# Optimization experiments

Measured on AMD Instinct MI355X. Metric: run time of the kernel, lower is better.

Reference implementation:

```python
import jax, jax.numpy as jnp
import numpy as np

EPS = 1e-6

def _phi(x):
    # elu(x) + 1 feature map
    return jax.nn.elu(x) + 1.0

def setup_inputs() -> dict:
    key = jax.random.key(0)
    kq, kk, kv = jax.random.split(key, 3)
    N, L, S, H, D, M = 8, 4096, 4096, 8, 64, 64
    queries = jax.random.normal(kq, (N, L, H, D), dtype=jnp.float32)
    keys = jax.random.normal(kk, (N, S, H, D), dtype=jnp.float32)
    values = jax.random.normal(kv, (N, S, H, M), dtype=jnp.float32)
    key_mask = jnp.ones((N, S), dtype=jnp.float32)  # key_lengths.float_matrix
    return {"queries": queries, "keys": keys, "values": values, "key_mask": key_mask}

def reference(queries, keys, values, key_mask):
    Q = _phi(queries)                                   # [N,L,H,D]
    K = _phi(keys) * key_mask[:, :, None, None]         # [N,S,H,D]
    KV = jnp.einsum('nshd,nshm->nhmd', K, values)       # [N,H,M,D]
    Z = 1.0 / (jnp.einsum('nlhd,nhd->nlh', Q, K.sum(axis=1)) + EPS)  # [N,L,H]
    V = jnp.einsum('nlhd,nhmd,nlh->nlhm', Q, KV, Z)     # [N,L,H,M]
    return V
```

## Files before the change

kernel.cpp:

```cpp
#include <hip/hip_runtime.h>


#define SLEN 4096
#define LLEN 4096
#define NHTOT 64
#define HD   512
#define NSPLIT 16
#define EPSF 1e-6f

__device__ __forceinline__ float phi(float x) {
    return x > 0.0f ? x + 1.0f : __expf(x);
}

__device__ __forceinline__ void fma4(float4& a, float s, const float4& b) {
    a.x = fmaf(s, b.x, a.x);
    a.y = fmaf(s, b.y, a.y);
    a.z = fmaf(s, b.z, a.z);
    a.w = fmaf(s, b.w, a.w);
}

__global__ __launch_bounds__(256)
void la_phase1(const float* __restrict__ Kg, const float* __restrict__ Vg,
               const float* __restrict__ maskg,
               float* __restrict__ KVp, float* __restrict__ Ksump) {
    __shared__ float kb[64 * 68];
    __shared__ float vb[64 * 64];
    __shared__ float ksb[16 * 64];

    const int tid  = threadIdx.x;
    const int w    = tid >> 6;
    const int lane = tid & 63;
    const int nh   = blockIdx.y;
    const int n    = nh >> 3;
    const int h    = nh & 7;
    const int sp   = blockIdx.x;

    const int sr = tid >> 4;
    const int c4 = (tid & 15) * 4;
    const int wd = w & 1, wm = w >> 1;
    const int d0 = wd * 32 + (lane & 7) * 4;
    const int m0 = wm * 32 + (lane >> 3) * 4;

    const size_t base = (size_t)n * SLEN * HD + (size_t)h * 64;
    const float* mrow = maskg + (size_t)n * SLEN;
    const int sblock = sp * 256;

    float4 acc[4];
    #pragma unroll
    for (int i = 0; i < 4; ++i) acc[i] = make_float4(0.f, 0.f, 0.f, 0.f);
    float4 ksp = make_float4(0.f, 0.f, 0.f, 0.f);

    for (int t = 0; t < 4; ++t) {
        const int srow0 = sblock + t * 64;
        __syncthreads();
        #pragma unroll
        for (int u = 0; u < 4; ++u) {
            const int row = sr + u * 16;
            const int s   = srow0 + row;
            const size_t g = base + (size_t)s * HD + c4;
            float4 kf = *(const float4*)(Kg + g);
            const float mm = mrow[s];
            kf.x = phi(kf.x) * mm;
            kf.y = phi(kf.y) * mm;
            kf.z = phi(kf.z) * mm;
            kf.w = phi(kf.w) * mm;
            ksp.x += kf.x; ksp.y += kf.y; ksp.z += kf.z; ksp.w += kf.w;
            *(float4*)&kb[row * 68 + c4] = kf;
            *(float4*)&vb[row * 64 + c4] = *(const float4*)(Vg + g);
        }
        __syncthreads();
        #pragma unroll 8
        for (int s = 0; s < 64; ++s) {
            const float4 k4 = *(const float4*)&kb[s * 68 + d0];
            const float4 v4 = *(const float4*)&vb[s * 64 + m0];
            fma4(acc[0], k4.x, v4);
            fma4(acc[1], k4.y, v4);
            fma4(acc[2], k4.z, v4);
            fma4(acc[3], k4.w, v4);
        }
    }

    float* outp = KVp + ((size_t)sp * NHTOT + nh) * 4096;
    #pragma unroll
    for (int di = 0; di < 4; ++di)
        *(float4*)&outp[(d0 + di) * 64 + m0] = acc[di];

    *(float4*)&ksb[sr * 64 + c4] = ksp;
    __syncthreads();
    if (tid < 64) {
        float ssum = 0.f;
        #pragma unroll
        for (int r = 0; r < 16; ++r) ssum += ksb[r * 64 + tid];
        Ksump[((size_t)sp * NHTOT + nh) * 64 + tid] = ssum;
    }
}

__global__ __launch_bounds__(256)
void la_reduce(const float* __restrict__ KVp, const float* __restrict__ Ksump,
               float* __restrict__ KVt, float* __restrict__ Ksum) {
    const int nh  = blockIdx.x;
    const int tid = threadIdx.x;
    #pragma unroll
    for (int j = 0; j < 4; ++j) {
        const int f = (j * 256 + tid) * 4;
        float4 a = make_float4(0.f, 0.f, 0.f, 0.f);
        #pragma unroll
        for (int s = 0; s < NSPLIT; ++s) {
            const float4 v = *(const float4*)&KVp[((size_t)s * NHTOT + nh) * 4096 + f];
            a.x += v.x; a.y += v.y; a.z += v.z; a.w += v.w;
        }
        *(float4*)&KVt[(size_t)nh * 4096 + f] = a;
    }
    if (tid < 64) {
        float a = 0.f;
        #pragma unroll
        for (int s = 0; s < NSPLIT; ++s)
            a += Ksump[((size_t)s * NHTOT + nh) * 64 + tid];
        Ksum[nh * 64 + tid] = a;
    }
}

__global__ __launch_bounds__(256)
void la_phase2(const float* __restrict__ Qg, const float* __restrict__ KVt,
               const float* __restrict__ Ksum, float* __restrict__ Og) {
    __shared__ float Qs[128 * 68];
    __shared__ float KVs[64 * 64];
    __shared__ float KSs[64];

    const int tid = threadIdx.x;
    const int nh  = blockIdx.y;
    const int n   = nh >> 3;
    const int h   = nh & 7;
    const int lbase = blockIdx.x * 128;

    #pragma unroll
    for (int j = 0; j < 4; ++j) {
        const int f = (j * 256 + tid) * 4;
        *(float4*)&KVs[f] = *(const float4*)&KVt[(size_t)nh * 4096 + f];
    }
    if (tid < 16) *(float4*)&KSs[tid * 4] = *(const float4*)&Ksum[nh * 64 + tid * 4];

    const int sr = tid >> 4;
    const int c4 = (tid & 15) * 4;
    #pragma unroll
    for (int u = 0; u < 8; ++u) {
        const int row = sr + u * 16;
        float4 q = *(const float4*)&Qg[((size_t)(n * LLEN + lbase + row) * 8 + h) * 64 + c4];
        q.x = phi(q.x); q.y = phi(q.y); q.z = phi(q.z); q.w = phi(q.w);
        *(float4*)&Qs[row * 68 + c4] = q;
    }
    __syncthreads();

    const int w    = tid >> 6;
    const int lane = tid & 63;
    const int ty   = lane >> 4;
    const int tx   = lane & 15;
    const int m0   = tx * 4;
    const int rb   = w * 32 + ty;

    float4 acc[8];
    float  den[8];
    #pragma unroll
    for (int i = 0; i < 8; ++i) {
        acc[i] = make_float4(0.f, 0.f, 0.f, 0.f);
        den[i] = 0.f;
    }

    for (int d4 = 0; d4 < 16; ++d4) {
        const float4 ks = *(const float4*)&KSs[d4 * 4];
        float4 q4[8];
        #pragma unroll
        for (int i = 0; i < 8; ++i)
            q4[i] = *(const float4*)&Qs[(rb + 4 * i) * 68 + d4 * 4];
        #pragma unroll
        for (int i = 0; i < 8; ++i) {
            den[i] = fmaf(q4[i].x, ks.x, den[i]);
            den[i] = fmaf(q4[i].y, ks.y, den[i]);
            den[i] = fmaf(q4[i].z, ks.z, den[i]);
            den[i] = fmaf(q4[i].w, ks.w, den[i]);
        }
        #pragma unroll
        for (int dk = 0; dk < 4; ++dk) {
            const float4 kv = *(const float4*)&KVs[(d4 * 4 + dk) * 64 + m0];
            #pragma unroll
            for (int i = 0; i < 8; ++i)
                fma4(acc[i], (&q4[i].x)[dk], kv);
        }
    }

    #pragma unroll
    for (int i = 0; i < 8; ++i) {
        const int l = lbase + rb + 4 * i;
        const float z = 1.0f / (den[i] + EPSF);
        float4 o = acc[i];
        o.x *= z; o.y *= z; o.z *= z; o.w *= z;
        *(float4*)&Og[((size_t)(n * LLEN + l) * 8 + h) * 64 + m0] = o;
    }
}

extern "C" void kernel_launch(void* const* d_in, const int* in_sizes, int n_in,
                              void* d_out, int out_size, void* d_ws, size_t ws_size,
                              hipStream_t stream) {
    const float* Q    = (const float*)d_in[0];
    const float* K    = (const float*)d_in[1];
    const float* V    = (const float*)d_in[2];
    const float* mask = (const float*)d_in[3];
    float* out = (float*)d_out;

    float* KVp   = (float*)d_ws;
    float* Ksump = KVp + (size_t)NSPLIT * NHTOT * 4096;
    float* KVt   = Ksump + (size_t)NSPLIT * NHTOT * 64;
    float* Ksum  = KVt + (size_t)NHTOT * 4096;

    dim3 g1(NSPLIT, NHTOT);
    la_phase1<<<g1, 256, 0, stream>>>(K, V, mask, KVp, Ksump);

    la_reduce<<<NHTOT, 256, 0, stream>>>(KVp, Ksump, KVt, Ksum);

    dim3 g2(LLEN / 128, NHTOT);
    la_phase2<<<g2, 256, 0, stream>>>(Q, KVt, Ksum, out);
}
```

Measured before the change: 255.1 us.

## Retile phase1 with per-wave S split and LDS reduction, widen reduce and phase2 tiles

Phase1 now has each wave own a 16-row slice of S and accumulate the full 64x64 KV tile with an 8x8 register block per thread. The four wave partials are combined through a two-step LDS tree reduction. The reduce kernel is flattened across 257 blocks so more of the GPU is busy. Phase2 processes 256 rows per block with 8x8 register tiles and a swizzled, half-depth Q staging buffer to cut LDS bank conflicts. The larger register tiles raise the FMA-per-load ratio but increase register pressure, and the phase2 grid shrinks to half as many blocks.

After: 292.0 us. +14.4%, slower.

```diff
diff --git a/kernel.cpp b/kernel.cpp
--- a/kernel.cpp
+++ b/kernel.cpp
@@ -19,13 +19,20 @@
     a.w = fmaf(s, b.w, a.w);
 }
 
+__device__ __forceinline__ void add4(float4& a, const float4& b) {
+    a.x += b.x; a.y += b.y; a.z += b.z; a.w += b.w;
+}
+
 __global__ __launch_bounds__(256)
 void la_phase1(const float* __restrict__ Kg, const float* __restrict__ Vg,
                const float* __restrict__ maskg,
                float* __restrict__ KVp, float* __restrict__ Ksump) {
-    __shared__ float kb[64 * 68];
-    __shared__ float vb[64 * 64];
-    __shared__ float ksb[16 * 64];
+    __shared__ float lds[9472];
+    float* kb  = lds;
+    float* vb  = lds + 4352;
+    float* ksb = lds + 8448;
+    float* Red0 = lds;
+    float* Red1 = lds + 4096;
 
     const int tid  = threadIdx.x;
     const int w    = tid >> 6;
@@ -37,17 +44,19 @@
 
     const int sr = tid >> 4;
     const int c4 = (tid & 15) * 4;
-    const int wd = w & 1, wm = w >> 1;
-    const int d0 = wd * 32 + (lane & 7) * 4;
-    const int m0 = wm * 32 + (lane >> 3) * 4;
+    const int d0 = (lane & 7) * 8;
+    const int m0 = (lane >> 3) * 8;
 
     const size_t base = (size_t)n * SLEN * HD + (size_t)h * 64;
     const float* mrow = maskg + (size_t)n * SLEN;
     const int sblock = sp * 256;
 
-    float4 acc[4];
+    float4 acc[8][2];
     #pragma unroll
-    for (int i = 0; i < 4; ++i) acc[i] = make_float4(0.f, 0.f, 0.f, 0.f);
+    for (int i = 0; i < 8; ++i) {
+        acc[i][0] = make_float4(0.f, 0.f, 0.f, 0.f);
+        acc[i][1] = make_float4(0.f, 0.f, 0.f, 0.f);
+    }
     float4 ksp = make_float4(0.f, 0.f, 0.f, 0.f);
 
     for (int t = 0; t < 4; ++t) {
@@ -69,69 +78,123 @@
             *(float4*)&vb[row * 64 + c4] = *(const float4*)(Vg + g);
         }
         __syncthreads();
-        #pragma unroll 8
-        for (int s = 0; s < 64; ++s) {
-            const float4 k4 = *(const float4*)&kb[s * 68 + d0];
-            const float4 v4 = *(const float4*)&vb[s * 64 + m0];
-            fma4(acc[0], k4.x, v4);
-            fma4(acc[1], k4.y, v4);
-            fma4(acc[2], k4.z, v4);
-            fma4(acc[3], k4.w, v4);
-        }
-    }
-
-    float* outp = KVp + ((size_t)sp * NHTOT + nh) * 4096;
-    #pragma unroll
-    for (int di = 0; di < 4; ++di)
-        *(float4*)&outp[(d0 + di) * 64 + m0] = acc[di];
-
+        #pragma unroll
+        for (int j = 0; j < 16; ++j) {
+            const int s = w * 16 + j;
+            const float4 ka = *(const float4*)&kb[s * 68 + d0];
+            const float4 kc = *(const float4*)&kb[s * 68 + d0 + 4];
+            const float4 va = *(const float4*)&vb[s * 64 + m0];
+            const float4 vc = *(const float4*)&vb[s * 64 + m0 + 4];
+            const float kk[8] = {ka.x, ka.y, ka.z, ka.w, kc.x, kc.y, kc.z, kc.w};
+            #pragma unroll
+            for (int di = 0; di < 8; ++di) {
+                fma4(acc[di][0], kk[di], va);
+                fma4(acc[di][1], kk[di], vc);
+            }
+        }
+    }
+
+    __syncthreads();
+    if (w == 2) {
+        #pragma unroll
+        for (int di = 0; di < 8; ++di) {
+            *(float4*)&Red0[(d0 + di) * 64 + m0]     = acc[di][0];
+            *(float4*)&Red0[(d0 + di) * 64 + m0 + 4] = acc[di][1];
+        }
+    }
+    if (w == 3) {
+        #pragma unroll
+        for (int di = 0; di < 8; ++di) {
+            *(float4*)&Red1[(d0 + di) * 64 + m0]     = acc[di][0];
+            *(float4*)&Red1[(d0 + di) * 64 + m0 + 4] = acc[di][1];
+        }
+    }
     *(float4*)&ksb[sr * 64 + c4] = ksp;
     __syncthreads();
+    if (w == 0) {
+        #pragma unroll
+        for (int di = 0; di < 8; ++di) {
+            const float4 a = *(const float4*)&Red0[(d0 + di) * 64 + m0];
+            const float4 b = *(const float4*)&Red0[(d0 + di) * 64 + m0 + 4];
+            add4(acc[di][0], a);
+            add4(acc[di][1], b);
+        }
+    }
+    if (w == 1) {
+        #pragma unroll
+        for (int di = 0; di < 8; ++di) {
+            const float4 a = *(const float4*)&Red1[(d0 + di) * 64 + m0];
+            const float4 b = *(const float4*)&Red1[(d0 + di) * 64 + m0 + 4];
+            add4(acc[di][0], a);
+            add4(acc[di][1], b);
+        }
+    }
     if (tid < 64) {
         float ssum = 0.f;
         #pragma unroll
         for (int r = 0; r < 16; ++r) ssum += ksb[r * 64 + tid];
         Ksump[((size_t)sp * NHTOT + nh) * 64 + tid] = ssum;
+    }
+    __syncthreads();
+    if (w == 1) {
+        #pragma unroll
+        for (int di = 0; di < 8; ++di) {
+            *(float4*)&Red0[(d0 + di) * 64 + m0]     = acc[di][0];
+            *(float4*)&Red0[(d0 + di) * 64 + m0 + 4] = acc[di][1];
+        }
+    }
+    __syncthreads();
+    if (w == 0) {
+        float* outp = KVp + ((size_t)sp * NHTOT + nh) * 4096;
+        #pragma unroll
+        for (int di = 0; di < 8; ++di) {
+            const float4 a = *(const float4*)&Red0[(d0 + di) * 64 + m0];
+            const float4 b = *(const float4*)&Red0[(d0 + di) * 64 + m0 + 4];
+            float4 o0 = acc[di][0], o1 = acc[di][1];
+            add4(o0, a);
+            add4(o1, b);
+            *(float4*)&outp[(d0 + di) * 64 + m0]     = o0;
+            *(float4*)&outp[(d0 + di) * 64 + m0 + 4] = o1;
+        }
     }
 }
 
 __global__ __launch_bounds__(256)
 void la_reduce(const float* __restrict__ KVp, const float* __restrict__ Ksump,
                float* __restrict__ KVt, float* __restrict__ Ksum) {
-    const int nh  = blockIdx.x;
     const int tid = threadIdx.x;
-    #pragma unroll
-    for (int j = 0; j < 4; ++j) {
-        const int f = (j * 256 + tid) * 4;
+    if (blockIdx.x < 256) {
+        const size_t f = ((size_t)blockIdx.x * 256 + tid) * 4;
         float4 a = make_float4(0.f, 0.f, 0.f, 0.f);
         #pragma unroll
-        for (int s = 0; s < NSPLIT; ++s) {
-            const float4 v = *(const float4*)&KVp[((size_t)s * NHTOT + nh) * 4096 + f];
-            a.x += v.x; a.y += v.y; a.z += v.z; a.w += v.w;
-        }
-        *(float4*)&KVt[(size_t)nh * 4096 + f] = a;
-    }
-    if (tid < 64) {
-        float a = 0.f;
-        #pragma unroll
-        for (int s = 0; s < NSPLIT; ++s)
-            a += Ksump[((size_t)s * NHTOT + nh) * 64 + tid];
-        Ksum[nh * 64 + tid] = a;
+        for (int sp = 0; sp < NSPLIT; ++sp)
+            add4(a, *(const float4*)&KVp[(size_t)sp * NHTOT * 4096 + f]);
+        *(float4*)&KVt[f] = a;
+    } else {
+        #pragma unroll
+        for (int j = 0; j < 4; ++j) {
+            const int c = (j * 256 + tid) * 4;
+            float4 a = make_float4(0.f, 0.f, 0.f, 0.f);
+            #pragma unroll
+            for (int sp = 0; sp < NSPLIT; ++sp)
+                add4(a, *(const float4*)&Ksump[sp * NHTOT * 64 + c]);
+            *(float4*)&Ksum[c] = a;
+        }
     }
 }
 
 __global__ __launch_bounds__(256)
 void la_phase2(const float* __restrict__ Qg, const float* __restrict__ KVt,
                const float* __restrict__ Ksum, float* __restrict__ Og) {
-    __shared__ float Qs[128 * 68];
-    __shared__ float KVs[64 * 64];
+    __shared__ float Qs[256 * 32];
+    __shared__ float KVs[4096];
     __shared__ float KSs[64];
 
     const int tid = threadIdx.x;
     const int nh  = blockIdx.y;
     const int n   = nh >> 3;
     const int h   = nh & 7;
-    const int lbase = blockIdx.x * 128;
+    const int lbase = blockIdx.x * 256;
 
     #pragma unroll
     for (int j = 0; j < 4; ++j) {
@@ -140,61 +203,79 @@
     }
     if (tid < 16) *(float4*)&KSs[tid * 4] = *(const float4*)&Ksum[nh * 64 + tid * 4];
 
-    const int sr = tid >> 4;
-    const int c4 = (tid & 15) * 4;
-    #pragma unroll
-    for (int u = 0; u < 8; ++u) {
-        const int row = sr + u * 16;
-        float4 q = *(const float4*)&Qg[((size_t)(n * LLEN + lbase + row) * 8 + h) * 64 + c4];
-        q.x = phi(q.x); q.y = phi(q.y); q.z = phi(q.z); q.w = phi(q.w);
-        *(float4*)&Qs[row * 68 + c4] = q;
-    }
-    __syncthreads();
-
     const int w    = tid >> 6;
     const int lane = tid & 63;
-    const int ty   = lane >> 4;
-    const int tx   = lane & 15;
-    const int m0   = tx * 4;
-    const int rb   = w * 32 + ty;
-
-    float4 acc[8];
+    const int ry   = lane >> 3;
+    const int tx   = lane & 7;
+    const int m0   = tx * 8;
+    const int rowb = w * 64 + ry;
+
+    const int sc   = tid & 7;
+    const int srow = tid >> 3;
+
+    float4 acc[8][2];
     float  den[8];
     #pragma unroll
     for (int i = 0; i < 8; ++i) {
-        acc[i] = make_float4(0.f, 0.f, 0.f, 0.f);
+        acc[i][0] = make_float4(0.f, 0.f, 0.f, 0.f);
+        acc[i][1] = make_float4(0.f, 0.f, 0.f, 0.f);
         den[i] = 0.f;
     }
 
-    for (int d4 = 0; d4 < 16; ++d4) {
-        const float4 ks = *(const float4*)&KSs[d4 * 4];
-        float4 q4[8];
-        #pragma unroll
-        for (int i = 0; i < 8; ++i)
-            q4[i] = *(const float4*)&Qs[(rb + 4 * i) * 68 + d4 * 4];
-        #pragma unroll
-        for (int i = 0; i < 8; ++i) {
-            den[i] = fmaf(q4[i].x, ks.x, den[i]);
-            den[i] = fmaf(q4[i].y, ks.y, den[i]);
-            den[i] = fmaf(q4[i].z, ks.z, den[i]);
-            den[i] = fmaf(q4[i].w, ks.w, den[i]);
-        }
-        #pragma unroll
-        for (int dk = 0; dk < 4; ++dk) {
-            const float4 kv = *(const float4*)&KVs[(d4 * 4 + dk) * 64 + m0];
-            #pragma unroll
-            for (int i = 0; i < 8; ++i)
-                fma4(acc[i], (&q4[i].x)[dk], kv);
+    for (int half = 0; half < 2; ++half) {
+        __syncthreads();
+        #pragma unroll
+        for (int p = 0; p < 8; ++p) {
+            const int row = srow + p * 32;
+            float4 q = *(const float4*)&Qg[((size_t)(n * LLEN + lbase + row) * 8 + h) * 64
+                                           + half * 32 + sc * 4];
+            q.x = phi(q.x); q.y = phi(q.y); q.z = phi(q.z); q.w = phi(q.w);
+            const int chunk = (sc + row) & 7;
+            *(float4*)&Qs[row * 32 + chunk * 4] = q;
+        }
+        __syncthreads();
+        #pragma unroll
+        for (int dq = 0; dq < 8; ++dq) {
+            const float4 ks = *(const float4*)&KSs[(half * 8 + dq) * 4];
+            float4 q4[8];
+            #pragma unroll
+            for (int i = 0; i < 8; ++i) {
+                const int row = rowb + 8 * i;
+                const int chunk = (dq + row) & 7;
+                q4[i] = *(const float4*)&Qs[row * 32 + chunk * 4];
+            }
+            #pragma unroll
+            for (int i = 0; i < 8; ++i) {
+                den[i] = fmaf(q4[i].x, ks.x, den[i]);
+                den[i] = fmaf(q4[i].y, ks.y, den[i]);
+                den[i] = fmaf(q4[i].z, ks.z, den[i]);
+                den[i] = fmaf(q4[i].w, ks.w, den[i]);
+            }
+            #pragma unroll
+            for (int dk = 0; dk < 4; ++dk) {
+                const int d = half * 32 + dq * 4 + dk;
+                const float4 kv0 = *(const float4*)&KVs[d * 64 + m0];
+                const float4 kv1 = *(const float4*)&KVs[d * 64 + m0 + 4];
+                #pragma unroll
+                for (int i = 0; i < 8; ++i) {
+                    const float qs = (&q4[i].x)[dk];
+                    fma4(acc[i][0], qs, kv0);
+                    fma4(acc[i][1], qs, kv1);
+                }
+            }
         }
     }
 
     #pragma unroll
     for (int i = 0; i < 8; ++i) {
-        const int l = lbase + rb + 4 * i;
+        const int l = lbase + rowb + 8 * i;
         const float z = 1.0f / (den[i] + EPSF);
-        float4 o = acc[i];
-        o.x *= z; o.y *= z; o.z *= z; o.w *= z;
-        *(float4*)&Og[((size_t)(n * LLEN + l) * 8 + h) * 64 + m0] = o;
+        float4 o0 = acc[i][0], o1 = acc[i][1];
+        o0.x *= z; o0.y *= z; o0.z *= z; o0.w *= z;
+        o1.x *= z; o1.y *= z; o1.z *= z; o1.w *= z;
+        float* op = Og + ((size_t)(n * LLEN + l) * 8 + h) * 64 + m0;
+        *(float4*)&op[0] = o0;
+        *(float4*)&op[4] = o1;
     }
 }
 
@@ -215,8 +296,8 @@
     dim3 g1(NSPLIT, NHTOT);
     la_phase1<<<g1, 256, 0, stream>>>(K, V, mask, KVp, Ksump);
 
-    la_reduce<<<NHTOT, 256, 0, stream>>>(KVp, Ksump, KVt, Ksum);
-
-    dim3 g2(LLEN / 128, NHTOT);
+    la_reduce<<<257, 256, 0, stream>>>(KVp, Ksump, KVt, Ksum);
+
+    dim3 g2(LLEN / 256, NHTOT);
     la_phase2<<<g2, 256, 0, stream>>>(Q, KVt, Ksum, out);
 }
```
